# Performance work log

Hardware: AMD Instinct MI355X
Metric: run time of the kernel (lower is better)

Reference implementation:

```python
import jax, jax.numpy as jnp
import numpy as np

NUM_HEADS = 12


def setup_inputs() -> dict:
    key = jax.random.key(0)
    k1, k2, k3 = jax.random.split(key, 3)
    B, T, N, D = 8, 8, 196, 768
    x = jax.random.normal(k1, (B, T * N, D), dtype=jnp.float32)
    w_qkv = jax.random.normal(k2, (D, 3 * D), dtype=jnp.float32) * 0.02
    w_proj = jax.random.normal(k3, (D, D), dtype=jnp.float32) * 0.02
    b_proj = jnp.zeros((D,), dtype=jnp.float32)
    return {"x": x, "T": T, "N": N, "w_qkv": w_qkv, "w_proj": w_proj, "b_proj": b_proj}


def reference(x, T, N, w_qkv, w_proj, b_proj):
    B, TN, D = x.shape
    H = NUM_HEADS
    hd = D // H
    scale = hd ** -0.5
    # qkv projection: (B, TN, 3, H, hd)
    qkv = (x @ w_qkv).reshape(B, TN, 3, H, hd)
    # -> (3, B, H, T, N, hd)
    qkv = jnp.transpose(qkv, (2, 0, 3, 1, 4)).reshape(3, B, H, T, N, hd)
    q, k, v = qkv[0], qkv[1], qkv[2]

    # Temporal branch: mean-pool over spatial axis N (keepdim -> length-1 attn axis)
    q_t = q.mean(axis=3, keepdims=True)            # (B,H,T,1,hd)
    k_t = k.mean(axis=3, keepdims=True)            # (B,H,T,1,hd)
    v_t = v.mean(axis=3, keepdims=True)            # (B,H,T,1,hd)
    attn_t = jnp.einsum('bhtqd,bhtkd->bhtqk', q_t, k_t) * scale  # (B,H,T,1,1)
    attn_t = jax.nn.softmax(attn_t, axis=-1)
    x_t = jnp.einsum('bhtqk,bhtkd->bhtqd', attn_t, v_t)[:, :, :, 0]  # (B,H,T,hd)

    # Spatial branch: full attention within each frame
    attn_s = jnp.einsum('bhtnd,bhtmd->bhtnm', q, k) * scale  # (B,H,T,N,N)
    attn_s = jax.nn.softmax(attn_s, axis=-1)
    x_s = jnp.einsum('bhtnm,bhtmd->bhtnd', attn_s, v)        # (B,H,T,N,hd)

    # Combine: broadcast temporal result over spatial positions, add
    out = x_s + x_t[:, :, :, None, :]                        # (B,H,T,N,hd)
    out = out.reshape(B, H, T * N, hd)
    out = jnp.transpose(out, (0, 2, 1, 3)).reshape(B * T * N, D)
    return out @ w_proj + b_proj
```

## Files before the change

### kernel.cpp

```cpp
#include <hip/hip_runtime.h>
#include <math.h>

#define BB 8
#define TT 8
#define NN 196
#define DD 768
#define HH 12
#define HD 64
#define TN (TT * NN)
#define MM (BB * TN)
#define D3 (3 * DD)

typedef _Float16 f16;
typedef _Float16 f16x8 __attribute__((ext_vector_type(8)));
typedef _Float16 f16x4 __attribute__((ext_vector_type(4)));
typedef float f32x4 __attribute__((ext_vector_type(4)));
typedef unsigned int u32;

#define GLDS16(gp, lp)                                                        \
  __builtin_amdgcn_global_load_lds(                                           \
      (const __attribute__((address_space(1))) u32*)(gp),                     \
      (__attribute__((address_space(3))) u32*)(lp), 16, 0, 0)

#define MFMA16(a, b, c) __builtin_amdgcn_mfma_f32_16x16x32_f16(a, b, c, 0, 0, 0)

__global__ __launch_bounds__(256) void gemm_f16nt(
    const f16* __restrict__ A, const f16* __restrict__ Bt,
    float* __restrict__ C32, f16* __restrict__ C16, int K, int Ncol,
    const float* __restrict__ bias, int mode) {
  __shared__ f16 As[128 * 64];
  __shared__ f16 Bs[128 * 64];

  const int tid = threadIdx.x;
  const int lane = tid & 63;
  const int wave = tid >> 6;
  const int wy = wave >> 1, wx = wave & 1;
  const int bm = blockIdx.y * 128;
  const int bn = blockIdx.x * 128;

  const f16* aP[4];
  const f16* bP[4];
#pragma unroll
  for (int it = 0; it < 4; it++) {
    int ci = tid + it * 256;
    int r = ci >> 3;
    int c = (ci & 7) ^ (r & 7);
    aP[it] = A + (size_t)(bm + r) * K + c * 8;
    bP[it] = Bt + (size_t)(bn + r) * K + c * 8;
  }

  f32x4 acc[4][4];
#pragma unroll
  for (int i = 0; i < 4; i++)
#pragma unroll
    for (int j = 0; j < 4; j++) acc[i][j] = (f32x4)0.0f;

  const int fr = lane & 15;
  const int q = lane >> 4;
  const int sw = fr & 7;

  for (int kt = 0; kt < K; kt += 64) {
#pragma unroll
    for (int it = 0; it < 4; it++) {
      GLDS16(aP[it] + kt, &As[(tid + it * 256) * 8]);
      GLDS16(bP[it] + kt, &Bs[(tid + it * 256) * 8]);
    }
    __syncthreads();

#pragma unroll
    for (int kk = 0; kk < 2; kk++) {
      const int lc = ((kk * 4 + q) ^ sw) * 8;
      f16x8 af[4], bf[4];
#pragma unroll
      for (int mi = 0; mi < 4; mi++)
        af[mi] = *(const f16x8*)&As[(wy * 64 + mi * 16 + fr) * 64 + lc];
#pragma unroll
      for (int ni = 0; ni < 4; ni++)
        bf[ni] = *(const f16x8*)&Bs[(wx * 64 + ni * 16 + fr) * 64 + lc];

#pragma unroll
      for (int mi = 0; mi < 4; mi++)
#pragma unroll
        for (int ni = 0; ni < 4; ni++)
          acc[mi][ni] = MFMA16(af[mi], bf[ni], acc[mi][ni]);
    }
    __syncthreads();
  }

  if (mode == 0) {
#pragma unroll
    for (int mi = 0; mi < 4; mi++) {
      const int row0 = bm + wy * 64 + mi * 16 + (lane >> 4) * 4;
#pragma unroll
      for (int ni = 0; ni < 4; ni++) {
        const int col = bn + wx * 64 + ni * 16 + (lane & 15);
        float bv = (bias != nullptr) ? bias[col] : 0.0f;
#pragma unroll
        for (int r = 0; r < 4; r++)
          C32[(size_t)(row0 + r) * Ncol + col] = acc[mi][ni][r] + bv;
      }
    }
  } else {
#pragma unroll
    for (int mi = 0; mi < 4; mi++) {
      const int row0 = bm + wy * 64 + mi * 16 + (lane >> 4) * 4;
#pragma unroll
      for (int r = 0; r < 4; r++) {
        const int token = row0 + r;
        const int f = token / NN;
        const int n = token - f * NN;
        f16* fb = C16 + ((size_t)f * (HH * 3) * NN) * 64 + n * 64;
#pragma unroll
        for (int ni = 0; ni < 4; ni++) {
          const int col = bn + wx * 64 + ni * 16 + (lane & 15);
          const int qt = col / DD;
          const int rem = col - qt * DD;
          const int hh = rem >> 6;
          const int d = rem & 63;
          fb[(size_t)(hh * 3 + qt) * NN * 64 + d] = (f16)acc[mi][ni][r];
        }
      }
    }
  }
}

__global__ __launch_bounds__(256) void conv_f32_to_f16(
    const float* __restrict__ in, f16* __restrict__ out, int n4) {
  int i = blockIdx.x * blockDim.x + threadIdx.x;
  const int stride = gridDim.x * blockDim.x;
  for (; i < n4; i += stride) {
    float4 f = ((const float4*)in)[i];
    f16x4 h;
    h[0] = (f16)f.x;
    h[1] = (f16)f.y;
    h[2] = (f16)f.z;
    h[3] = (f16)f.w;
    ((f16x4*)out)[i] = h;
  }
}

__global__ __launch_bounds__(256) void transpose_f32_to_f16(
    const float* __restrict__ W, f16* __restrict__ Wt, int K, int Ncol) {
  __shared__ float tileS[32][33];
  const int k0 = blockIdx.y * 32, n0 = blockIdx.x * 32;
  const int tx = threadIdx.x & 31, ty = threadIdx.x >> 5;
#pragma unroll
  for (int i = 0; i < 4; i++)
    tileS[ty + i * 8][tx] = W[(size_t)(k0 + ty + i * 8) * Ncol + n0 + tx];
  __syncthreads();
#pragma unroll
  for (int i = 0; i < 4; i++)
    Wt[(size_t)(n0 + ty + i * 8) * K + k0 + tx] = (f16)tileS[tx][ty + i * 8];
}

#define VSTR 232

__global__ __launch_bounds__(512, 4) void attn_mfma(
    const f16* __restrict__ qkv, f16* __restrict__ out) {
  __shared__ f16 KS[196 * 64];
  __shared__ f16 VS[64 * VSTR];
  __shared__ __align__(16) f16 PS[8 * 16 * 40];
  __shared__ float vmean[64];
  float* red = (float*)PS;

  const int bi = blockIdx.x;
  const int t = bi % TT;
  const int h = (bi / TT) % HH;
  const int b = bi / (TT * HH);
  const int frame = b * TT + t;
  const int tok0 = frame * NN;

  const f16* Qb = qkv + (size_t)(frame * HH + h) * 3 * NN * 64;
  const f16* Kb = Qb + NN * 64;
  const f16* Vb = Qb + 2 * NN * 64;

  const int tid = threadIdx.x;
  const int lane = tid & 63;
  const int wave = tid >> 6;
  const int m = lane & 15;
  const int q = lane >> 4;

#pragma unroll
  for (int it = 0; it < 3; it++) {
    int chunk = tid + it * 512;
    int row = chunk >> 3, pc = chunk & 7;
    int c = pc ^ (row & 7);
    GLDS16(Kb + row * 64 + c * 8, &KS[chunk * 8]);
  }
  if (tid < 32) {
    int chunk = 1536 + tid;
    int row = chunk >> 3, pc = chunk & 7;
    int c = pc ^ (row & 7);
    *(f16x8*)&KS[chunk * 8] = *(const f16x8*)(Kb + row * 64 + c * 8);
  }

  for (int idx = tid; idx < 64 * 9; idx += 512) {
    int d = idx / 9, c = idx % 9;
    *(f16x4*)&VS[d * VSTR + 196 + c * 4] = (f16x4){0, 0, 0, 0};
  }

  const int vd = tid & 63;
  const int kb = tid >> 6;
  float vpart = 0.0f;
  if (kb < 7) {
#pragma unroll
    for (int it = 0; it < 7; it++) {
      int k0 = kb * 28 + it * 4;
      f16x4 pk;
#pragma unroll
      for (int j = 0; j < 4; j++) {
        f16 v = Vb[(k0 + j) * 64 + vd];
        pk[j] = v;
        vpart += (float)v;
      }
      *(f16x4*)&VS[vd * VSTR + k0] = pk;
    }
  }
  red[tid] = vpart;
  __syncthreads();
  if (tid < 64) {
    float s = 0.0f;
#pragma unroll
    for (int g = 0; g < 8; g++) s += red[tid + 64 * g];
    vmean[tid] = s * (1.0f / (float)NN);
  }
  __syncthreads();

  f16* PSw = &PS[wave * 640];

  for (int qt = wave; qt < 13; qt += 8) {
    const int q0 = qt * 16;
    int qrow = q0 + m;
    if (qrow > NN - 1) qrow = NN - 1;
    const f16* qbase = Qb + qrow * 64;
    f16x8 aq0 = *(const f16x8*)(qbase + q * 8);
    f16x8 aq1 = *(const f16x8*)(qbase + 32 + q * 8);

    f32x4 o0 = (f32x4)0.0f, o1 = (f32x4)0.0f, o2 = (f32x4)0.0f,
          o3 = (f32x4)0.0f;
    float l[4] = {0.0f, 0.0f, 0.0f, 0.0f};

    for (int ch = 0; ch < 7; ch++) {
      const int keyA = ch * 32 + m;
      const int keyB = keyA + 16;
      const int kA = keyA > 195 ? 195 : keyA;
      const int kB = keyB > 195 ? 195 : keyB;
      const int swA = kA & 7, swB = kB & 7;
      f16x8 b00 = *(const f16x8*)&KS[kA * 64 + ((q ^ swA) * 8)];
      f16x8 b01 = *(const f16x8*)&KS[kA * 64 + (((q + 4) ^ swA) * 8)];
      f16x8 b10 = *(const f16x8*)&KS[kB * 64 + ((q ^ swB) * 8)];
      f16x8 b11 = *(const f16x8*)&KS[kB * 64 + (((q + 4) ^ swB) * 8)];
      f32x4 z = (f32x4)0.0f;
      f32x4 s0 = MFMA16(aq0, b00, z);
      s0 = MFMA16(aq1, b01, s0);
      f32x4 s1 = MFMA16(aq0, b10, z);
      s1 = MFMA16(aq1, b11, s1);

      const bool v0 = keyA < NN;
      const bool v1 = keyB < NN;
#pragma unroll
      for (int r = 0; r < 4; r++) {
        float p0 = v0 ? __expf(s0[r] * 0.125f) : 0.0f;
        float p1 = v1 ? __expf(s1[r] * 0.125f) : 0.0f;
        l[r] += p0 + p1;
        PSw[(q * 4 + r) * 40 + m] = (f16)p0;
        PSw[(q * 4 + r) * 40 + 16 + m] = (f16)p1;
      }
      f16x8 pa = *(const f16x8*)&PSw[m * 40 + q * 8];
      f16x8 bv0 = *(const f16x8*)&VS[(0 * 16 + m) * VSTR + ch * 32 + q * 8];
      f16x8 bv1 = *(const f16x8*)&VS[(1 * 16 + m) * VSTR + ch * 32 + q * 8];
      f16x8 bv2 = *(const f16x8*)&VS[(2 * 16 + m) * VSTR + ch * 32 + q * 8];
      f16x8 bv3 = *(const f16x8*)&VS[(3 * 16 + m) * VSTR + ch * 32 + q * 8];
      o0 = MFMA16(pa, bv0, o0);
      o1 = MFMA16(pa, bv1, o1);
      o2 = MFMA16(pa, bv2, o2);
      o3 = MFMA16(pa, bv3, o3);
    }

#pragma unroll
    for (int r = 0; r < 4; r++) {
      float s = l[r];
      s += __shfl_xor(s, 1);
      s += __shfl_xor(s, 2);
      s += __shfl_xor(s, 4);
      s += __shfl_xor(s, 8);
      l[r] = 1.0f / s;
    }

#pragma unroll
    for (int r = 0; r < 4; r++) {
      const int query = q0 + q * 4 + r;
      if (query < NN) {
        f16* orow = out + (size_t)(tok0 + query) * DD + h * HD;
        orow[m] = (f16)(o0[r] * l[r] + vmean[m]);
        orow[16 + m] = (f16)(o1[r] * l[r] + vmean[16 + m]);
        orow[32 + m] = (f16)(o2[r] * l[r] + vmean[32 + m]);
        orow[48 + m] = (f16)(o3[r] * l[r] + vmean[48 + m]);
      }
    }
  }
}

extern "C" void kernel_launch(void* const* d_in, const int* in_sizes, int n_in,
                              void* d_out, int out_size, void* d_ws,
                              size_t ws_size, hipStream_t stream) {
  (void)in_sizes;
  (void)n_in;
  (void)out_size;
  (void)ws_size;
  const float* x      = (const float*)d_in[0];
  const float* w_qkv  = (const float*)d_in[3];
  const float* w_proj = (const float*)d_in[4];
  const float* b_proj = (const float*)d_in[5];
  float* out = (float*)d_out;

  char* ws = (char*)d_ws;
  f16* qkvh = (f16*)ws;
  f16* xh = (f16*)(ws + (size_t)MM * D3 * 2);
  f16* wqkvT = xh + (size_t)MM * DD;
  f16* wprojT = wqkvT + (size_t)D3 * DD;

  conv_f32_to_f16<<<2048, 256, 0, stream>>>(x, xh, MM * DD / 4);
  transpose_f32_to_f16<<<dim3(D3 / 32, DD / 32), 256, 0, stream>>>(w_qkv,
                                                                   wqkvT, DD, D3);
  transpose_f32_to_f16<<<dim3(DD / 32, DD / 32), 256, 0, stream>>>(w_proj,
                                                                   wprojT, DD, DD);
  gemm_f16nt<<<dim3(D3 / 128, MM / 128), 256, 0, stream>>>(
      xh, wqkvT, nullptr, qkvh, DD, D3, nullptr, 1);
  attn_mfma<<<BB * HH * TT, 512, 0, stream>>>(qkvh, xh);
  gemm_f16nt<<<dim3(DD / 128, MM / 128), 256, 0, stream>>>(
      xh, wprojT, out, nullptr, DD, DD, b_proj, 0);
}
```

Before: 232.3 us.

## Replace QKV GEMM with 256x256 tile, 8-wave pipelined kernel and XCD swizzle

Adds a dedicated QKV projection GEMM that uses 256x256 output tiles with 512 threads and double-buffered LDS loaded via global_load_lds. It interleaves the prefetch stages with MFMA quadrants behind explicit barriers and priority hints. Workgroup IDs are remapped so neighbouring tiles land on the same XCD. The larger tile raises arithmetic intensity and data reuse relative to the old 128x128 kernel, but it uses 128KB of LDS per block and has a complex schedule that depends on exact waitcnt counts.

```diff
diff --git a/kernel.cpp b/kernel.cpp
--- a/kernel.cpp
+++ b/kernel.cpp
@@ -23,6 +23,177 @@
       (__attribute__((address_space(3))) u32*)(lp), 16, 0, 0)
 
 #define MFMA16(a, b, c) __builtin_amdgcn_mfma_f32_16x16x32_f16(a, b, c, 0, 0, 0)
+#define SBAR() __builtin_amdgcn_s_barrier()
+#define SCHED() __builtin_amdgcn_sched_barrier(0)
+#define PBAR()  do { SCHED(); SBAR(); SCHED(); } while (0)
+
+#define GK DD
+#define GNT 12
+
+template <int MI0, int NJ0>
+__device__ __forceinline__ void quad(f32x4 (&acc)[8][4],
+                                     const f16x8 (&af)[4][2],
+                                     const f16x8 (&bf)[2][2]) {
+  __builtin_amdgcn_s_setprio(1);
+#pragma unroll
+  for (int i = 0; i < 4; i++)
+#pragma unroll
+    for (int j = 0; j < 2; j++) {
+      acc[MI0 + i][NJ0 + j] = MFMA16(af[i][0], bf[j][0], acc[MI0 + i][NJ0 + j]);
+      acc[MI0 + i][NJ0 + j] = MFMA16(af[i][1], bf[j][1], acc[MI0 + i][NJ0 + j]);
+    }
+  __builtin_amdgcn_s_setprio(0);
+}
+
+__global__ __launch_bounds__(512, 2) void gemm256_qkv(
+    const f16* __restrict__ A, const f16* __restrict__ Bt,
+    f16* __restrict__ C16) {
+  __shared__ f16 As[2 * 256 * 64];
+  __shared__ f16 Bs[2 * 256 * 64];
+
+  const int nwg = 49 * 9;
+  const int orig = blockIdx.x;
+  const int xcd = orig & 7;
+  const int inner = orig >> 3;
+  const int qq = nwg >> 3;
+  const int rr = nwg & 7;
+  const int swzid =
+      ((xcd < rr) ? xcd * (qq + 1) : rr * (qq + 1) + (xcd - rr) * qq) + inner;
+  const int bm = (swzid / 9) * 256;
+  const int bn = (swzid % 9) * 256;
+
+  const int tid = threadIdx.x;
+  const int lane = tid & 63;
+  const int wave = tid >> 6;
+  const int wy = wave >> 2;
+  const int wx = wave & 3;
+  const int m = lane & 15;
+  const int q = lane >> 4;
+
+  const int sr = tid >> 3;
+  const int sc = (tid & 7) ^ (sr & 7);
+  const f16* gA = A + (size_t)(bm + sr) * GK + sc * 8;
+  const f16* gB = Bt + (size_t)(bn + sr) * GK + sc * 8;
+  f16* lA = &As[tid * 8];
+  f16* lB = &Bs[tid * 8];
+
+#define STAGE_A(db, h, tile)                                   \
+  do {                                                         \
+    const f16* _s = gA + (size_t)(h) * 128 * GK + (tile) * 64; \
+    f16* _d = lA + (db) * 16384 + (h) * 8192;                  \
+    GLDS16(_s, _d);                                            \
+    GLDS16(_s + 64 * GK, _d + 4096);                           \
+  } while (0)
+#define STAGE_B(db, h, tile)                                   \
+  do {                                                         \
+    const f16* _s = gB + (size_t)(h) * 128 * GK + (tile) * 64; \
+    f16* _d = lB + (db) * 16384 + (h) * 8192;                  \
+    GLDS16(_s, _d);                                            \
+    GLDS16(_s + 64 * GK, _d + 4096);                           \
+  } while (0)
+
+  const int sw = m & 7;
+  const int c0 = (q ^ sw) * 8;
+  const int c1 = ((q + 4) ^ sw) * 8;
+  const f16* rA = &As[(wy * 128 + m) * 64];
+  const f16* rB = &Bs[(wx * 64 + m) * 64];
+
+  STAGE_A(0, 0, 0);
+  STAGE_A(0, 1, 0);
+  STAGE_B(0, 0, 0);
+  STAGE_B(0, 1, 0);
+  STAGE_B(1, 0, 1);
+  STAGE_B(1, 1, 1);
+
+  f32x4 acc[8][4];
+#pragma unroll
+  for (int i = 0; i < 8; i++)
+#pragma unroll
+    for (int j = 0; j < 4; j++) acc[i][j] = (f32x4)0.0f;
+
+  SCHED();
+  asm volatile("s_waitcnt vmcnt(4)" ::: "memory");
+  SCHED();
+  SBAR();
+  SCHED();
+
+#pragma unroll 2
+  for (int t = 0; t < GNT; ++t) {
+    const int db = t & 1;
+    const f16* pA = rA + db * 16384;
+    const f16* pB = rB + db * 16384;
+    const int tA = (t + 1 < GNT) ? t + 1 : GNT - 1;
+    const int tB = (t + 2 < GNT) ? t + 2 : GNT - 1;
+
+    f16x8 af[4][2], bf0[2][2], bf1[2][2];
+
+#pragma unroll
+    for (int i = 0; i < 4; i++) {
+      af[i][0] = *(const f16x8*)(pA + i * 1024 + c0);
+      af[i][1] = *(const f16x8*)(pA + i * 1024 + c1);
+    }
+#pragma unroll
+    for (int j = 0; j < 2; j++) {
+      bf0[j][0] = *(const f16x8*)(pB + j * 1024 + c0);
+      bf0[j][1] = *(const f16x8*)(pB + j * 1024 + c1);
+    }
+    STAGE_A(db ^ 1, 0, tA);
+    PBAR();
+    quad<0, 0>(acc, af, bf0);
+    PBAR();
+
+#pragma unroll
+    for (int j = 0; j < 2; j++) {
+      bf1[j][0] = *(const f16x8*)(pB + (2 + j) * 1024 + c0);
+      bf1[j][1] = *(const f16x8*)(pB + (2 + j) * 1024 + c1);
+    }
+    STAGE_A(db ^ 1, 1, tA);
+    PBAR();
+    quad<0, 2>(acc, af, bf1);
+    PBAR();
+
+#pragma unroll
+    for (int i = 0; i < 4; i++) {
+      af[i][0] = *(const f16x8*)(pA + (4 + i) * 1024 + c0);
+      af[i][1] = *(const f16x8*)(pA + (4 + i) * 1024 + c1);
+    }
+    STAGE_B(db, 0, tB);
+    PBAR();
+    quad<4, 2>(acc, af, bf1);
+    PBAR();
+
+    STAGE_B(db, 1, tB);
+    SCHED();
+    asm volatile("s_waitcnt vmcnt(4)" ::: "memory");
+    PBAR();
+    quad<4, 0>(acc, af, bf0);
+    PBAR();
+  }
+
+  const int col0 = bn + wx * 64;
+#pragma unroll
+  for (int mi = 0; mi < 8; mi++) {
+    const int row0 = bm + wy * 128 + mi * 16 + q * 4;
+#pragma unroll
+    for (int r = 0; r < 4; r++) {
+      const int token = row0 + r;
+      const int f = token / NN;
+      const int n = token - f * NN;
+      f16* fb = C16 + ((size_t)f * (HH * 3)) * (NN * 64) + n * 64;
+#pragma unroll
+      for (int ni = 0; ni < 4; ni++) {
+        const int col = col0 + ni * 16 + m;
+        const int qt = col / DD;
+        const int rem = col - qt * DD;
+        const int hh = rem >> 6;
+        const int d = rem & 63;
+        fb[(size_t)(hh * 3 + qt) * (NN * 64) + d] = (f16)acc[mi][ni][r];
+      }
+    }
+  }
+#undef STAGE_A
+#undef STAGE_B
+}
 
 __global__ __launch_bounds__(256) void gemm_f16nt(
     const f16* __restrict__ A, const f16* __restrict__ Bt,
@@ -325,8 +496,7 @@
                                                                    wqkvT, DD, D3);
   transpose_f32_to_f16<<<dim3(DD / 32, DD / 32), 256, 0, stream>>>(w_proj,
                                                                    wprojT, DD, DD);
-  gemm_f16nt<<<dim3(D3 / 128, MM / 128), 256, 0, stream>>>(
-      xh, wqkvT, nullptr, qkvh, DD, D3, nullptr, 1);
+  gemm256_qkv<<<dim3(49 * 9), 512, 0, stream>>>(xh, wqkvT, qkvh);
   attn_mfma<<<BB * HH * TT, 512, 0, stream>>>(qkvh, xh);
   gemm_f16nt<<<dim3(DD / 128, MM / 128), 256, 0, stream>>>(
       xh, wprojT, out, nullptr, DD, DD, b_proj, 0);
```

Measured after the change: 215.0 us. -7.4%, faster.
